# Optimization experiments

Hardware: AMD Instinct MI355X
Metric: run time of the kernel (lower is better)

## Reference

```python
import jax, jax.numpy as jnp
import numpy as np
import math

B, N = 1, 512
C_S, C_Z, C_H, H = 384, 128, 16, 12
P_Q, P_V, NBINS = 4, 8, 64
OUT_DIM = H * (C_H + P_V * 4 + C_Z)


def setup_inputs() -> dict:
    key = jax.random.key(0)
    ks = jax.random.split(key, 16)
    def rn(k, shape, scale=1.0):
        return jax.random.normal(k, shape, dtype=jnp.float32) * scale
    rotations, _ = jnp.linalg.qr(rn(ks[3], (B, N, 3, 3)))  # orthogonal frames
    w = 0.02
    return {
        "s": rn(ks[0], (B, N, C_S)),
        "z": rn(ks[1], (B, N, N, C_Z)),
        "translations": rn(ks[2], (B, N, 3), 10.0),  # spread over ~0-32 A bins
        "rotations": rotations,
        "Wq": rn(ks[4], (C_S, H * C_H), w), "bq": jnp.zeros((H * C_H,), jnp.float32),
        "Wk": rn(ks[5], (C_S, H * C_H), w), "bk": jnp.zeros((H * C_H,), jnp.float32),
        "Wv": rn(ks[6], (C_S, H * C_H), w), "bv": jnp.zeros((H * C_H,), jnp.float32),
        "Wqp": rn(ks[7], (C_S, H * P_Q * 3), w), "bqp": jnp.zeros((H * P_Q * 3,), jnp.float32),
        "Wkp": rn(ks[8], (C_S, H * P_Q * 3), w), "bkp": jnp.zeros((H * P_Q * 3,), jnp.float32),
        "Wvp": rn(ks[9], (C_S, H * P_V * 3), w), "bvp": jnp.zeros((H * P_V * 3,), jnp.float32),
        "Wb": rn(ks[10], (C_Z, H), w), "bb": jnp.zeros((H,), jnp.float32),
        "emb": rn(ks[11], (NBINS, H), w),
        "scale_logits": jnp.zeros((3, H), jnp.float32),
        "head_weights": jnp.ones((H,), jnp.float32),
        "Wout": rn(ks[12], (OUT_DIM, C_S), w), "bout": jnp.zeros((C_S,), jnp.float32),
    }


def reference(s, z, translations, rotations, Wq, bq, Wk, bk, Wv, bv, Wqp, bqp, Wkp, bkp, Wvp, bvp, Wb, bb, emb, scale_logits, head_weights, Wout, bout):
    b, n, _ = s.shape
    t = translations
    q = (s @ Wq + bq).reshape(b, n, H, C_H)
    k = (s @ Wk + bk).reshape(b, n, H, C_H)
    v = (s @ Wv + bv).reshape(b, n, H, C_H)
    q_pts = (s @ Wqp + bqp).reshape(b, n, H, P_Q, 3)
    k_pts = (s @ Wkp + bkp).reshape(b, n, H, P_Q, 3)
    v_pts = (s @ Wvp + bvp).reshape(b, n, H, P_V, 3)
    # local -> global frame
    q_g = jnp.einsum('bnij,bnhpj->bnhpi', rotations, q_pts) + t[:, :, None, None, :]
    k_g = jnp.einsum('bnij,bnhpj->bnhpi', rotations, k_pts) + t[:, :, None, None, :]
    v_g = jnp.einsum('bnij,bnhpj->bnhpi', rotations, v_pts) + t[:, :, None, None, :]
    scalar_logits = jnp.einsum('bnhc,bmhc->bnmh', q, k) / math.sqrt(C_H)  # [b,n,m,h]
    point_dist = jnp.sum((q_g[:, :, None] - k_g[:, None]) ** 2, axis=-1)  # [b,n,m,h,p]
    point_logits = -0.5 * jnp.sum(point_dist, axis=-1) * head_weights[None, None, None, :]
    pair_bias = z @ Wb + bb  # [b,n,m,h]
    pair_dist = jnp.linalg.norm(t[:, :, None, :] - t[:, None, :, :], axis=-1)  # [b,n,m]
    edges = jnp.linspace(0.0, 32.0, NBINS + 1)
    bins = jnp.clip(jnp.searchsorted(edges, pair_dist, side='left') - 1, 0, NBINS - 1)
    dist_bias = emb[bins]  # [b,n,m,h]
    scales = jnp.stack([
        (pair_dist <= 5.0).astype(s.dtype),
        ((pair_dist > 5.0) & (pair_dist <= 15.0)).astype(s.dtype),
        jnp.ones_like(pair_dist),
    ], axis=-1)  # [b,n,m,3]
    per_head = jax.nn.softmax(scale_logits, axis=0)  # [3,h]
    multiscale = jnp.einsum('bnms,sh->bnmh', scales, per_head)
    logits = scalar_logits + point_logits + pair_bias + dist_bias + multiscale
    attn = jax.nn.softmax(logits.astype(jnp.float32), axis=2).astype(s.dtype)  # over m
    out_scalar = jnp.einsum('bnmh,bmhc->bnhc', attn, v)
    out_pts_g = jnp.einsum('bnmh,bmhpi->bnhpi', attn, v_g)
    # global -> local frame (R^T applied)
    out_pts_l = jnp.einsum('bnji,bnhpj->bnhpi', rotations, out_pts_g - t[:, :, None, None, :])
    out_norms = jnp.linalg.norm(out_pts_l, axis=-1)  # [b,n,h,p]
    pair_feat = jnp.einsum('bnmh,bnmc->bnhc', attn, z)
    feats = jnp.concatenate([
        out_scalar,
        out_pts_l.reshape(b, n, H, P_V * 3),
        out_norms,
        pair_feat,
    ], axis=-1).reshape(b, n, -1)  # [b,n,OUT_DIM]
    return feats @ Wout + bout
```

## Files before the change

kernel.cpp:

```cpp
#include <hip/hip_runtime.h>

#define NTOK 512
#define CS 384
#define CZ 128
#define CH 16
#define HN 12
#define PQ 4
#define PV 8
#define FEAT_DIM 2112
#define HSEG 176

__global__ __launch_bounds__(256) void k_proj(
    const float* __restrict__ s,
    const float* __restrict__ Wq,  const float* __restrict__ bq,
    const float* __restrict__ Wk,  const float* __restrict__ bk,
    const float* __restrict__ Wv,  const float* __restrict__ bv,
    const float* __restrict__ Wqp, const float* __restrict__ bqp,
    const float* __restrict__ Wkp, const float* __restrict__ bkp,
    const float* __restrict__ Wvp, const float* __restrict__ bvp,
    float* __restrict__ qs, float* __restrict__ ksT, float* __restrict__ vs,
    float* __restrict__ raw_g)
{
    __shared__ float s_l[16 * CS];
    __shared__ float Ws[16][64];
    const int t  = threadIdx.x;
    const int n0 = blockIdx.x * 16;

    const float4* sg  = (const float4*)(s + (size_t)n0 * CS);
    float4*       sl4 = (float4*)s_l;
#pragma unroll
    for (int j = 0; j < 6; ++j) sl4[j * 256 + t] = sg[j * 256 + t];

    const int col = blockIdx.y * 64 + (t & 63);
    const int tq  = t >> 6;
    const float* bv_;
    int lc;
    if (col < 192)      { bv_ = bq;  lc = col;       }
    else if (col < 384) { bv_ = bk;  lc = col - 192; }
    else if (col < 576) { bv_ = bv;  lc = col - 384; }
    else if (col < 720) { bv_ = bqp; lc = col - 576; }
    else if (col < 864) { bv_ = bkp; lc = col - 720; }
    else                { bv_ = bvp; lc = col - 864; }

    const int kk_s = t >> 4, cq = t & 15;
    const int gcol = blockIdx.y * 64 + cq * 4;
    const float* Wsrc; int lcs, ncs;
    if (gcol < 192)      { Wsrc = Wq;  lcs = gcol;       ncs = 192; }
    else if (gcol < 384) { Wsrc = Wk;  lcs = gcol - 192; ncs = 192; }
    else if (gcol < 576) { Wsrc = Wv;  lcs = gcol - 384; ncs = 192; }
    else if (gcol < 720) { Wsrc = Wqp; lcs = gcol - 576; ncs = 144; }
    else if (gcol < 864) { Wsrc = Wkp; lcs = gcol - 720; ncs = 144; }
    else                 { Wsrc = Wvp; lcs = gcol - 864; ncs = 288; }

    float a0, a1, a2, a3;
    a0 = a1 = a2 = a3 = bv_[lc];
    __syncthreads();

    for (int ks = 0; ks < CS; ks += 16) {
        float4 w4 = *(const float4*)&Wsrc[(size_t)(ks + kk_s) * ncs + lcs];
        __syncthreads();
        *(float4*)&Ws[kk_s][cq * 4] = w4;
        __syncthreads();
        const float* srow = s_l + tq * 4 * CS + ks;
#pragma unroll
        for (int kk = 0; kk < 16; ++kk) {
            float w = Ws[kk][t & 63];
            a0 += srow[kk] * w;
            a1 += srow[CS + kk] * w;
            a2 += srow[2 * CS + kk] * w;
            a3 += srow[3 * CS + kk] * w;
        }
    }

    const int n = n0 + tq * 4;
    if (col < 192) {
        qs[(size_t)(n + 0) * 192 + lc] = a0;
        qs[(size_t)(n + 1) * 192 + lc] = a1;
        qs[(size_t)(n + 2) * 192 + lc] = a2;
        qs[(size_t)(n + 3) * 192 + lc] = a3;
    } else if (col < 384) {
        float* p = ksT + (size_t)lc * NTOK + n;
        p[0] = a0; p[1] = a1; p[2] = a2; p[3] = a3;
    } else if (col < 576) {
        vs[(size_t)(n + 0) * 192 + lc] = a0;
        vs[(size_t)(n + 1) * 192 + lc] = a1;
        vs[(size_t)(n + 2) * 192 + lc] = a2;
        vs[(size_t)(n + 3) * 192 + lc] = a3;
    } else {
        const int pc = col - 576;
        raw_g[(size_t)(n + 0) * 576 + pc] = a0;
        raw_g[(size_t)(n + 1) * 576 + pc] = a1;
        raw_g[(size_t)(n + 2) * 576 + pc] = a2;
        raw_g[(size_t)(n + 3) * 576 + pc] = a3;
    }
}

__global__ __launch_bounds__(256) void k_frame(
    const float* __restrict__ raw_g,
    const float* __restrict__ trans,
    const float* __restrict__ rot,
    float* __restrict__ qg, float* __restrict__ kgT, float* __restrict__ vg,
    float* __restrict__ transT)
{
    const int e = blockIdx.x * 256 + threadIdx.x;
    if (e < 512 * 576) {
        const int n = e / 576, loc = e % 576;
        const int i = loc % 3, base = loc - i;
        const float* rp = raw_g + (size_t)n * 576 + base;
        float x0 = rp[0], x1 = rp[1], x2 = rp[2];
        const float* R = rot + (size_t)n * 9 + i * 3;
        float v = trans[(size_t)n * 3 + i] + R[0] * x0 + R[1] * x1 + R[2] * x2;
        if (loc < 144)      qg[(size_t)n * 144 + loc] = v;
        else if (loc < 288) kgT[(size_t)(loc - 144) * NTOK + n] = v;
        else                vg[(size_t)n * 288 + loc - 288] = v;
    } else {
        const int idx = e - 512 * 576;
        if (idx < 3 * NTOK) {
            const int m = idx / 3, i = idx % 3;
            transT[(size_t)i * NTOK + m] = trans[(size_t)m * 3 + i];
        }
    }
}

__global__ __launch_bounds__(256, 2) void k_mid(
    const float* __restrict__ z,
    const float* __restrict__ qs, const float* __restrict__ ksT,
    const float* __restrict__ qg, const float* __restrict__ kgT,
    const float* __restrict__ trans, const float* __restrict__ transT,
    const float* __restrict__ Wb, const float* __restrict__ bbv,
    const float* __restrict__ emb, const float* __restrict__ slog,
    const float* __restrict__ hw,
    float* __restrict__ attn, float* __restrict__ feats)
{
    __shared__ __align__(16) float lgT[NTOK * HN];
    __shared__ __align__(16) float zl[64 * 132];
    __shared__ __align__(16) float wbT[HN * CZ];
    __shared__ float embl[64 * HN];
    __shared__ float ql[192];
    __shared__ float qgl[144];
    __shared__ float tl[3];
    __shared__ float phl[36];
    __shared__ float hwl[HN];

    const int n = blockIdx.x, t = threadIdx.x;

    for (int i = t; i < CZ * HN; i += 256) {
        const int h = i >> 7, c = i & 127;
        wbT[h * CZ + c] = Wb[(size_t)c * HN + h];
    }
    for (int i = t; i < 64 * HN; i += 256) embl[i] = emb[i];
    if (t < 192) ql[t] = qs[(size_t)n * 192 + t];
    if (t < 144) qgl[t] = qg[(size_t)n * 144 + t];
    if (t < 3)   tl[t] = trans[(size_t)n * 3 + t];
    if (t < HN)  hwl[t] = hw[t];
    if (t >= 64 && t < 64 + HN) {
        const int h = t - 64;
        float s0 = slog[h], s1 = slog[HN + h], s2 = slog[2 * HN + h];
        float mx = fmaxf(s0, fmaxf(s1, s2));
        float e0 = expf(s0 - mx), e1 = expf(s1 - mx), e2 = expf(s2 - mx);
        float inv = 1.f / (e0 + e1 + e2);
        phl[h] = e0 * inv; phl[12 + h] = e1 * inv; phl[24 + h] = e2 * inv;
    }

    const int ml = t & 63, hg = t >> 6, h0 = hg * 3;
    const float bb0 = bbv[h0], bb1 = bbv[h0 + 1], bb2 = bbv[h0 + 2];

    const float* w0 = wbT + (h0 + 0) * CZ;
    const float* w1 = wbT + (h0 + 1) * CZ;
    const float* w2 = wbT + (h0 + 2) * CZ;

    for (int mc = 0; mc < 8; ++mc) {
        __syncthreads();
        {
            const float4* zg = (const float4*)(z + ((size_t)n * NTOK + mc * 64) * CZ);
#pragma unroll
            for (int j = 0; j < 8; ++j) {
                float4 v = zg[j * 256 + t];
                const int f = j * 256 + t;
                const int row = f >> 5, c4 = (f & 31) * 4;
                *(float4*)&zl[row * 132 + c4] = v;
            }
        }
        __syncthreads();

        const int mg = mc * 64 + ml;
        float b0 = bb0, b1 = bb1, b2 = bb2;
        const float* zrow = zl + ml * 132;
#pragma unroll 4
        for (int cq = 0; cq < CZ; cq += 4) {
            float4 zv = *(const float4*)&zrow[cq];
            float4 v0 = *(const float4*)&w0[cq];
            float4 v1 = *(const float4*)&w1[cq];
            float4 v2 = *(const float4*)&w2[cq];
            b0 += zv.x * v0.x + zv.y * v0.y + zv.z * v0.z + zv.w * v0.w;
            b1 += zv.x * v1.x + zv.y * v1.y + zv.z * v1.z + zv.w * v1.w;
            b2 += zv.x * v2.x + zv.y * v2.y + zv.z * v2.z + zv.w * v2.w;
        }
        float dx = tl[0] - transT[mg];
        float dy = tl[1] - transT[NTOK + mg];
        float dz = tl[2] - transT[2 * NTOK + mg];
        float dist = sqrtf(dx * dx + dy * dy + dz * dz);
        int bin = min(63, max(0, (int)ceilf(dist * 2.f) - 1));
        const float in5  = (dist <= 5.f) ? 1.f : 0.f;
        const float in15 = (dist > 5.f && dist <= 15.f) ? 1.f : 0.f;

        float acc[3] = {b0, b1, b2};
#pragma unroll
        for (int k = 0; k < 3; ++k) {
            const int h = h0 + k;
            float sc = 0.f;
            const float* kk = ksT + (size_t)h * CH * NTOK + mg;
            const float* qq = ql + h * CH;
#pragma unroll
            for (int c = 0; c < CH; ++c) sc += qq[c] * kk[(size_t)c * NTOK];
            float sd = 0.f;
            const float* kg = kgT + (size_t)h * 12 * NTOK + mg;
            const float* qp = qgl + h * 12;
#pragma unroll
            for (int i = 0; i < 12; ++i) {
                float d = qp[i] - kg[(size_t)i * NTOK];
                sd += d * d;
            }
            acc[k] += sc * 0.25f - 0.5f * sd * hwl[h]
                    + embl[bin * HN + h]
                    + phl[24 + h] + in5 * phl[h] + in15 * phl[12 + h];
        }
        lgT[mg * HN + h0 + 0] = acc[0];
        lgT[mg * HN + h0 + 1] = acc[1];
        lgT[mg * HN + h0 + 2] = acc[2];
    }
    __syncthreads();

    const int lane = t & 63;
#pragma unroll
    for (int hh = 0; hh < 3; ++hh) {
        const int h = h0 + hh;
        float v[8];
        float mx = -1e30f;
#pragma unroll
        for (int i = 0; i < 8; ++i) {
            v[i] = lgT[(lane + 64 * i) * HN + h];
            mx = fmaxf(mx, v[i]);
        }
#pragma unroll
        for (int off = 32; off; off >>= 1) mx = fmaxf(mx, __shfl_xor(mx, off));
        float sm = 0.f;
#pragma unroll
        for (int i = 0; i < 8; ++i) { v[i] = expf(v[i] - mx); sm += v[i]; }
#pragma unroll
        for (int off = 32; off; off >>= 1) sm += __shfl_xor(sm, off);
        const float inv = 1.f / sm;
        float* arow = attn + ((size_t)n * HN + h) * NTOK;
#pragma unroll
        for (int i = 0; i < 8; ++i) {
            float a = v[i] * inv;
            lgT[(lane + 64 * i) * HN + h] = a;
            arow[lane + 64 * i] = a;
        }
    }
    __syncthreads();

    const int slab = t >> 6;
    const int c2 = (t & 63) * 2;
    float pacc[HN][2];
#pragma unroll
    for (int h = 0; h < HN; ++h) { pacc[h][0] = 0.f; pacc[h][1] = 0.f; }
    const float* zp = z + (size_t)n * NTOK * CZ + (size_t)slab * 128 * CZ + c2;
    const float* lp = lgT + slab * 128 * HN;
#pragma unroll 4
    for (int m = 0; m < 128; ++m) {
        float2 zv = *(const float2*)(zp + (size_t)m * CZ);
        float4 a0 = *(const float4*)&lp[m * HN + 0];
        float4 a1 = *(const float4*)&lp[m * HN + 4];
        float4 a2 = *(const float4*)&lp[m * HN + 8];
        pacc[0][0]  += a0.x * zv.x;  pacc[0][1]  += a0.x * zv.y;
        pacc[1][0]  += a0.y * zv.x;  pacc[1][1]  += a0.y * zv.y;
        pacc[2][0]  += a0.z * zv.x;  pacc[2][1]  += a0.z * zv.y;
        pacc[3][0]  += a0.w * zv.x;  pacc[3][1]  += a0.w * zv.y;
        pacc[4][0]  += a1.x * zv.x;  pacc[4][1]  += a1.x * zv.y;
        pacc[5][0]  += a1.y * zv.x;  pacc[5][1]  += a1.y * zv.y;
        pacc[6][0]  += a1.z * zv.x;  pacc[6][1]  += a1.z * zv.y;
        pacc[7][0]  += a1.w * zv.x;  pacc[7][1]  += a1.w * zv.y;
        pacc[8][0]  += a2.x * zv.x;  pacc[8][1]  += a2.x * zv.y;
        pacc[9][0]  += a2.y * zv.x;  pacc[9][1]  += a2.y * zv.y;
        pacc[10][0] += a2.z * zv.x;  pacc[10][1] += a2.z * zv.y;
        pacc[11][0] += a2.w * zv.x;  pacc[11][1] += a2.w * zv.y;
    }
    float* out_l = zl;
    for (int s = 0; s < 4; ++s) {
        __syncthreads();
        if (slab == s) {
#pragma unroll
            for (int h = 0; h < HN; ++h) {
                float* p = &out_l[h * CZ + c2];
                if (s == 0) { p[0] = pacc[h][0]; p[1] = pacc[h][1]; }
                else        { p[0] += pacc[h][0]; p[1] += pacc[h][1]; }
            }
        }
    }
    __syncthreads();
    for (int i = t; i < HN * CZ; i += 256) {
        const int h = i >> 7, c = i & 127;
        feats[(size_t)n * FEAT_DIM + h * HSEG + 48 + c] = out_l[i];
    }
}

__global__ __launch_bounds__(256) void k_outmm(
    const float* __restrict__ attn,
    const float* __restrict__ vs, const float* __restrict__ vg,
    const float* __restrict__ trans,
    const float* __restrict__ rot,
    float* __restrict__ feats)
{
    __shared__ float As_t[64][33];
    __shared__ float Vs[64][40];
    __shared__ float out_l[32 * 40];
    __shared__ float Rl[32][9];
    __shared__ float tl[32][3];
    const int t   = threadIdx.x;
    const int gn0 = blockIdx.x * 32;
    const int h   = blockIdx.y;

    const int slab  = t >> 6;
    const int w     = t & 63;
    const int n0l   = (w >> 3) * 4;
    const int j0    = (w & 7) * 5;

    float acc[4][5];
#pragma unroll
    for (int i = 0; i < 4; ++i)
#pragma unroll
        for (int k = 0; k < 5; ++k) acc[i][k] = 0.f;

    for (int step = 0; step < 8; ++step) {
        const int mb = step * 64;
        __syncthreads();
#pragma unroll
        for (int jj = 0; jj < 2; ++jj) {
            const int f = t + jj * 256;
            const int n_loc = f >> 4, c4 = f & 15;
            float4 a = *(const float4*)&attn[(((size_t)(gn0 + n_loc)) * HN + h) * NTOK + mb + c4 * 4];
            As_t[c4 * 4 + 0][n_loc] = a.x;
            As_t[c4 * 4 + 1][n_loc] = a.y;
            As_t[c4 * 4 + 2][n_loc] = a.z;
            As_t[c4 * 4 + 3][n_loc] = a.w;
        }
#pragma unroll
        for (int jj = 0; jj < 10; ++jj) {
            const int f = t + jj * 256;
            const int m_loc = f / 40, jv = f % 40;
            float v;
            if (jv < 16) v = vs[(size_t)(mb + m_loc) * 192 + h * 16 + jv];
            else         v = vg[(size_t)(mb + m_loc) * 288 + h * 24 + (jv - 16)];
            Vs[m_loc][jv] = v;
        }
        __syncthreads();
#pragma unroll
        for (int mi = 0; mi < 16; ++mi) {
            const int m = slab * 16 + mi;
            float4 a = *(const float4*)&As_t[m][n0l];
            float vv[5];
#pragma unroll
            for (int k = 0; k < 5; ++k) vv[k] = Vs[m][j0 + k];
            const float av[4] = {a.x, a.y, a.z, a.w};
#pragma unroll
            for (int i = 0; i < 4; ++i)
#pragma unroll
                for (int k = 0; k < 5; ++k)
                    acc[i][k] += av[i] * vv[k];
        }
    }

    for (int s = 0; s < 4; ++s) {
        __syncthreads();
        if (slab == s) {
#pragma unroll
            for (int i = 0; i < 4; ++i)
#pragma unroll
                for (int k = 0; k < 5; ++k) {
                    float* p = &out_l[(n0l + i) * 40 + j0 + k];
                    if (s == 0) *p = acc[i][k];
                    else        *p += acc[i][k];
                }
        }
    }
    for (int i = t; i < 32 * 12; i += 256) {
        const int n_loc = i / 12, r = i % 12;
        if (r < 9) Rl[n_loc][r] = rot[(size_t)(gn0 + n_loc) * 9 + r];
        else       tl[n_loc][r - 9] = trans[(size_t)(gn0 + n_loc) * 3 + (r - 9)];
    }
    __syncthreads();

    for (int f = t; f < 32 * 48; f += 256) {
        const int n_loc = f / 48, j = f % 48;
        const float* sh = &out_l[n_loc * 40];
        float* fp = feats + (size_t)(gn0 + n_loc) * FEAT_DIM + h * HSEG;
        const float* R = Rl[n_loc];
        const float* tv = tl[n_loc];
        if (j < 16) {
            fp[j] = sh[j];
        } else if (j < 40) {
            const int jj = j - 16, p = jj / 3, i = jj % 3;
            float val = 0.f;
#pragma unroll
            for (int q = 0; q < 3; ++q) val += R[q * 3 + i] * (sh[16 + p * 3 + q] - tv[q]);
            fp[16 + jj] = val;
        } else {
            const int p = j - 40;
            float s2 = 0.f;
#pragma unroll
            for (int i = 0; i < 3; ++i) {
                float val = 0.f;
#pragma unroll
                for (int q = 0; q < 3; ++q) val += R[q * 3 + i] * (sh[16 + p * 3 + q] - tv[q]);
                s2 += val * val;
            }
            fp[40 + p] = sqrtf(s2);
        }
    }
}

#define KT 16
__global__ __launch_bounds__(256) void k_outproj(
    const float* __restrict__ feats,
    const float* __restrict__ Wout,
    const float* __restrict__ bout,
    float* __restrict__ out)
{
    __shared__ float As[KT][64];
    __shared__ float Bs[KT][64];
    const int t  = threadIdx.x;
    const int n0 = blockIdx.x * 64;
    const int j0 = blockIdx.y * 64;
    const int k0 = blockIdx.z * HSEG;

    const int arow = t >> 2, akq = (t & 3) * 4;
    const int bkk  = t >> 4, bjq = (t & 15) * 4;
    const int tr   = t >> 4, tc  = t & 15;

    float acc[4][4] = {{0.f}};
    for (int s = 0; s < 11; ++s) {
        const int ks = k0 + s * KT;
        float4 a4 = *(const float4*)&feats[(size_t)(n0 + arow) * FEAT_DIM + ks + akq];
        float4 b4 = *(const float4*)&Wout[(size_t)(ks + bkk) * 384 + j0 + bjq];
        __syncthreads();
        As[akq + 0][arow] = a4.x;
        As[akq + 1][arow] = a4.y;
        As[akq + 2][arow] = a4.z;
        As[akq + 3][arow] = a4.w;
        *(float4*)&Bs[bkk][bjq] = b4;
        __syncthreads();
#pragma unroll
        for (int kk = 0; kk < KT; ++kk) {
            float4 av = *(const float4*)&As[kk][tr * 4];
            float4 bv = *(const float4*)&Bs[kk][tc * 4];
            acc[0][0] += av.x * bv.x; acc[0][1] += av.x * bv.y;
            acc[0][2] += av.x * bv.z; acc[0][3] += av.x * bv.w;
            acc[1][0] += av.y * bv.x; acc[1][1] += av.y * bv.y;
            acc[1][2] += av.y * bv.z; acc[1][3] += av.y * bv.w;
            acc[2][0] += av.z * bv.x; acc[2][1] += av.z * bv.y;
            acc[2][2] += av.z * bv.z; acc[2][3] += av.z * bv.w;
            acc[3][0] += av.w * bv.x; acc[3][1] += av.w * bv.y;
            acc[3][2] += av.w * bv.z; acc[3][3] += av.w * bv.w;
        }
    }

    const bool addb = (blockIdx.z == 0);
#pragma unroll
    for (int i = 0; i < 4; ++i) {
        const int row = n0 + tr * 4 + i;
#pragma unroll
        for (int jj = 0; jj < 4; ++jj) {
            const int col = j0 + tc * 4 + jj;
            float v = acc[i][jj];
            if (addb) v += bout[col];
            atomicAdd(&out[(size_t)row * 384 + col], v);
        }
    }
}

extern "C" void kernel_launch(void* const* d_in, const int* in_sizes, int n_in,
                              void* d_out, int out_size, void* d_ws, size_t ws_size,
                              hipStream_t stream) {
    const float* s     = (const float*)d_in[0];
    const float* z     = (const float*)d_in[1];
    const float* trans = (const float*)d_in[2];
    const float* rot   = (const float*)d_in[3];
    const float* Wq    = (const float*)d_in[4];
    const float* bq    = (const float*)d_in[5];
    const float* Wk    = (const float*)d_in[6];
    const float* bk    = (const float*)d_in[7];
    const float* Wv    = (const float*)d_in[8];
    const float* bv    = (const float*)d_in[9];
    const float* Wqp   = (const float*)d_in[10];
    const float* bqp   = (const float*)d_in[11];
    const float* Wkp   = (const float*)d_in[12];
    const float* bkp   = (const float*)d_in[13];
    const float* Wvp   = (const float*)d_in[14];
    const float* bvp   = (const float*)d_in[15];
    const float* Wb    = (const float*)d_in[16];
    const float* bb    = (const float*)d_in[17];
    const float* emb   = (const float*)d_in[18];
    const float* slog  = (const float*)d_in[19];
    const float* hw    = (const float*)d_in[20];
    const float* Wout  = (const float*)d_in[21];
    const float* bout  = (const float*)d_in[22];

    float* W = (float*)d_ws;
    float* qs     = W;
    float* ksT    = qs + 98304;
    float* vs     = ksT + 98304;
    float* qg     = vs + 98304;
    float* kgT    = qg + 73728;
    float* vg     = kgT + 73728;
    float* transT = vg + 147456;
    float* attn   = transT + 1536;
    float* feats  = attn + 3145728;
    float* raw_g  = feats + 1081344;

    k_proj<<<dim3(32, 18), 256, 0, stream>>>(s, Wq, bq, Wk, bk, Wv, bv,
                                             Wqp, bqp, Wkp, bkp, Wvp, bvp,
                                             qs, ksT, vs, raw_g);
    k_frame<<<1158, 256, 0, stream>>>(raw_g, trans, rot, qg, kgT, vg, transT);
    k_mid<<<512, 256, 0, stream>>>(z, qs, ksT, qg, kgT, trans, transT,
                                   Wb, bb, emb, slog, hw, attn, feats);
    k_outmm<<<dim3(16, 12), 256, 0, stream>>>(attn, vs, vg, trans, rot, feats);
    hipMemsetAsync(d_out, 0, (size_t)NTOK * 384 * sizeof(float), stream);
    k_outproj<<<dim3(8, 6, 12), 256, 0, stream>>>(feats, Wout, bout, (float*)d_out);
}
```

Measured before the change: 384.1 us.

## Process two keys per thread in k_mid and keep logits in registers

The k_mid kernel now stages 128 z rows per chunk (four chunks instead of eight) and each thread computes logits for two adjacent keys, so every weight float4 read from shared memory is reused twice and the ksT/kgT/transT loads become float2. Logits stay in registers for the softmax instead of passing through a separate lgT shared array, and attention values are written into the reused z staging buffer. This cuts shared-memory traffic, barriers and loop overhead, but raises register pressure under the launch bound of two blocks per SM, and the larger z tile keeps shared-memory use about the same.

```diff
diff --git a/kernel.cpp b/kernel.cpp
--- a/kernel.cpp
+++ b/kernel.cpp
@@ -132,8 +132,7 @@
     const float* __restrict__ hw,
     float* __restrict__ attn, float* __restrict__ feats)
 {
-    __shared__ __align__(16) float lgT[NTOK * HN];
-    __shared__ __align__(16) float zl[64 * 132];
+    __shared__ __align__(16) float zl[128 * 132];
     __shared__ __align__(16) float wbT[HN * CZ];
     __shared__ float embl[64 * HN];
     __shared__ float ql[192];
@@ -143,6 +142,7 @@
     __shared__ float hwl[HN];
 
     const int n = blockIdx.x, t = threadIdx.x;
+    const int ml = t & 63, hg = t >> 6, h0 = hg * 3;
 
     for (int i = t; i < CZ * HN; i += 256) {
         const int h = i >> 7, c = i & 127;
@@ -162,19 +162,20 @@
         phl[h] = e0 * inv; phl[12 + h] = e1 * inv; phl[24 + h] = e2 * inv;
     }
 
-    const int ml = t & 63, hg = t >> 6, h0 = hg * 3;
     const float bb0 = bbv[h0], bb1 = bbv[h0 + 1], bb2 = bbv[h0 + 2];
-
     const float* w0 = wbT + (h0 + 0) * CZ;
     const float* w1 = wbT + (h0 + 1) * CZ;
     const float* w2 = wbT + (h0 + 2) * CZ;
 
-    for (int mc = 0; mc < 8; ++mc) {
+    float lgr[3][8];
+
+#pragma unroll
+    for (int mc = 0; mc < 4; ++mc) {
         __syncthreads();
         {
-            const float4* zg = (const float4*)(z + ((size_t)n * NTOK + mc * 64) * CZ);
-#pragma unroll
-            for (int j = 0; j < 8; ++j) {
+            const float4* zg = (const float4*)(z + ((size_t)n * NTOK + mc * 128) * CZ);
+#pragma unroll
+            for (int j = 0; j < 16; ++j) {
                 float4 v = zg[j * 256 + t];
                 const int f = j * 256 + t;
                 const int row = f >> 5, c4 = (f & 31) * 4;
@@ -183,90 +184,112 @@
         }
         __syncthreads();
 
-        const int mg = mc * 64 + ml;
-        float b0 = bb0, b1 = bb1, b2 = bb2;
-        const float* zrow = zl + ml * 132;
+        const int m0 = mc * 128 + 2 * ml;
+        float b00 = bb0, b10 = bb1, b20 = bb2;
+        float b01 = bb0, b11 = bb1, b21 = bb2;
+        const float* zr0 = zl + (2 * ml) * 132;
+        const float* zr1 = zr0 + 132;
 #pragma unroll 4
-        for (int cq = 0; cq < CZ; cq += 4) {
-            float4 zv = *(const float4*)&zrow[cq];
-            float4 v0 = *(const float4*)&w0[cq];
-            float4 v1 = *(const float4*)&w1[cq];
-            float4 v2 = *(const float4*)&w2[cq];
-            b0 += zv.x * v0.x + zv.y * v0.y + zv.z * v0.z + zv.w * v0.w;
-            b1 += zv.x * v1.x + zv.y * v1.y + zv.z * v1.z + zv.w * v1.w;
-            b2 += zv.x * v2.x + zv.y * v2.y + zv.z * v2.z + zv.w * v2.w;
-        }
-        float dx = tl[0] - transT[mg];
-        float dy = tl[1] - transT[NTOK + mg];
-        float dz = tl[2] - transT[2 * NTOK + mg];
-        float dist = sqrtf(dx * dx + dy * dy + dz * dz);
-        int bin = min(63, max(0, (int)ceilf(dist * 2.f) - 1));
-        const float in5  = (dist <= 5.f) ? 1.f : 0.f;
-        const float in15 = (dist > 5.f && dist <= 15.f) ? 1.f : 0.f;
-
-        float acc[3] = {b0, b1, b2};
+        for (int cq = 0; cq < 32; ++cq) {
+            float4 z0 = *(const float4*)&zr0[cq * 4];
+            float4 z1 = *(const float4*)&zr1[cq * 4];
+            float4 v0 = *(const float4*)&w0[cq * 4];
+            float4 v1 = *(const float4*)&w1[cq * 4];
+            float4 v2 = *(const float4*)&w2[cq * 4];
+            b00 += z0.x * v0.x + z0.y * v0.y + z0.z * v0.z + z0.w * v0.w;
+            b10 += z0.x * v1.x + z0.y * v1.y + z0.z * v1.z + z0.w * v1.w;
+            b20 += z0.x * v2.x + z0.y * v2.y + z0.z * v2.z + z0.w * v2.w;
+            b01 += z1.x * v0.x + z1.y * v0.y + z1.z * v0.z + z1.w * v0.w;
+            b11 += z1.x * v1.x + z1.y * v1.y + z1.z * v1.z + z1.w * v1.w;
+            b21 += z1.x * v2.x + z1.y * v2.y + z1.z * v2.z + z1.w * v2.w;
+        }
+        float2 tx = *(const float2*)&transT[m0];
+        float2 ty = *(const float2*)&transT[NTOK + m0];
+        float2 tz = *(const float2*)&transT[2 * NTOK + m0];
+        float dx0 = tl[0] - tx.x, dy0 = tl[1] - ty.x, dz0 = tl[2] - tz.x;
+        float dx1 = tl[0] - tx.y, dy1 = tl[1] - ty.y, dz1 = tl[2] - tz.y;
+        float dist0 = sqrtf(dx0 * dx0 + dy0 * dy0 + dz0 * dz0);
+        float dist1 = sqrtf(dx1 * dx1 + dy1 * dy1 + dz1 * dz1);
+        int bin0 = min(63, max(0, (int)ceilf(dist0 * 2.f) - 1));
+        int bin1 = min(63, max(0, (int)ceilf(dist1 * 2.f) - 1));
+        const float in5_0  = (dist0 <= 5.f) ? 1.f : 0.f;
+        const float in15_0 = (dist0 > 5.f && dist0 <= 15.f) ? 1.f : 0.f;
+        const float in5_1  = (dist1 <= 5.f) ? 1.f : 0.f;
+        const float in15_1 = (dist1 > 5.f && dist1 <= 15.f) ? 1.f : 0.f;
+
+        float bk0[3] = {b00, b10, b20};
+        float bk1[3] = {b01, b11, b21};
 #pragma unroll
         for (int k = 0; k < 3; ++k) {
             const int h = h0 + k;
-            float sc = 0.f;
-            const float* kk = ksT + (size_t)h * CH * NTOK + mg;
+            float sc0 = 0.f, sc1 = 0.f;
+            const float* kk = ksT + (size_t)h * CH * NTOK + m0;
             const float* qq = ql + h * CH;
 #pragma unroll
-            for (int c = 0; c < CH; ++c) sc += qq[c] * kk[(size_t)c * NTOK];
-            float sd = 0.f;
-            const float* kg = kgT + (size_t)h * 12 * NTOK + mg;
+            for (int c = 0; c < CH; ++c) {
+                float2 kv = *(const float2*)&kk[(size_t)c * NTOK];
+                float q = qq[c];
+                sc0 += q * kv.x;
+                sc1 += q * kv.y;
+            }
+            float sd0 = 0.f, sd1 = 0.f;
+            const float* kg = kgT + (size_t)h * 12 * NTOK + m0;
             const float* qp = qgl + h * 12;
 #pragma unroll
             for (int i = 0; i < 12; ++i) {
-                float d = qp[i] - kg[(size_t)i * NTOK];
-                sd += d * d;
+                float2 gv = *(const float2*)&kg[(size_t)i * NTOK];
+                float q = qp[i];
+                float d0 = q - gv.x, d1 = q - gv.y;
+                sd0 += d0 * d0;
+                sd1 += d1 * d1;
             }
-            acc[k] += sc * 0.25f - 0.5f * sd * hwl[h]
-                    + embl[bin * HN + h]
-                    + phl[24 + h] + in5 * phl[h] + in15 * phl[12 + h];
-        }
-        lgT[mg * HN + h0 + 0] = acc[0];
-        lgT[mg * HN + h0 + 1] = acc[1];
-        lgT[mg * HN + h0 + 2] = acc[2];
+            const float hwv = hwl[h];
+            lgr[k][mc * 2 + 0] = bk0[k] + sc0 * 0.25f - 0.5f * sd0 * hwv
+                               + embl[bin0 * HN + h]
+                               + phl[24 + h] + in5_0 * phl[h] + in15_0 * phl[12 + h];
+            lgr[k][mc * 2 + 1] = bk1[k] + sc1 * 0.25f - 0.5f * sd1 * hwv
+                               + embl[bin1 * HN + h]
+                               + phl[24 + h] + in5_1 * phl[h] + in15_1 * phl[12 + h];
+        }
     }
     __syncthreads();
 
-    const int lane = t & 63;
+    float* attn_l = zl;
+    float* out_l  = zl + 8192;
 #pragma unroll
     for (int hh = 0; hh < 3; ++hh) {
         const int h = h0 + hh;
+        float mx = lgr[hh][0];
+#pragma unroll
+        for (int i = 1; i < 8; ++i) mx = fmaxf(mx, lgr[hh][i]);
+#pragma unroll
+        for (int off = 32; off; off >>= 1) mx = fmaxf(mx, __shfl_xor(mx, off));
         float v[8];
-        float mx = -1e30f;
-#pragma unroll
-        for (int i = 0; i < 8; ++i) {
-            v[i] = lgT[(lane + 64 * i) * HN + h];
-            mx = fmaxf(mx, v[i]);
-        }
-#pragma unroll
-        for (int off = 32; off; off >>= 1) mx = fmaxf(mx, __shfl_xor(mx, off));
         float sm = 0.f;
 #pragma unroll
-        for (int i = 0; i < 8; ++i) { v[i] = expf(v[i] - mx); sm += v[i]; }
+        for (int i = 0; i < 8; ++i) { v[i] = expf(lgr[hh][i] - mx); sm += v[i]; }
 #pragma unroll
         for (int off = 32; off; off >>= 1) sm += __shfl_xor(sm, off);
         const float inv = 1.f / sm;
         float* arow = attn + ((size_t)n * HN + h) * NTOK;
 #pragma unroll
-        for (int i = 0; i < 8; ++i) {
-            float a = v[i] * inv;
-            lgT[(lane + 64 * i) * HN + h] = a;
-            arow[lane + 64 * i] = a;
+        for (int mc = 0; mc < 4; ++mc) {
+            float a0 = v[mc * 2] * inv, a1 = v[mc * 2 + 1] * inv;
+            float2 a2; a2.x = a0; a2.y = a1;
+            *(float2*)&arow[mc * 128 + 2 * ml] = a2;
+            attn_l[(mc * 128 + 2 * ml) * HN + h] = a0;
+            attn_l[(mc * 128 + 2 * ml + 1) * HN + h] = a1;
         }
     }
     __syncthreads();
 
-    const int slab = t >> 6;
-    const int c2 = (t & 63) * 2;
+    const int slab = hg;
+    const int c2 = ml * 2;
     float pacc[HN][2];
 #pragma unroll
     for (int h = 0; h < HN; ++h) { pacc[h][0] = 0.f; pacc[h][1] = 0.f; }
     const float* zp = z + (size_t)n * NTOK * CZ + (size_t)slab * 128 * CZ + c2;
-    const float* lp = lgT + slab * 128 * HN;
+    const float* lp = attn_l + slab * 128 * HN;
 #pragma unroll 4
     for (int m = 0; m < 128; ++m) {
         float2 zv = *(const float2*)(zp + (size_t)m * CZ);
@@ -286,7 +309,6 @@
         pacc[10][0] += a2.z * zv.x;  pacc[10][1] += a2.z * zv.y;
         pacc[11][0] += a2.w * zv.x;  pacc[11][1] += a2.w * zv.y;
     }
-    float* out_l = zl;
     for (int s = 0; s < 4; ++s) {
         __syncthreads();
         if (slab == s) {
```

Measured after the change: 637.6 us. 66.0% more time.
